# Kernel tuning notes

Measured on AMD Instinct MI355X. Metric: run time of the kernel, lower is better.

The kernel has to match this reference:

```python
import jax, jax.numpy as jnp
import numpy as np
import math

B, S, D, H, HD = 2, 2048, 2048, 16, 128
ROPE_THETA = 10000.0


def _rope_cache(seq_len, dim, base, dtype=jnp.float32):
    inv_freq = 1.0 / (base ** (jnp.arange(0, dim, 2, dtype=jnp.float32) / dim))
    t = jnp.arange(seq_len, dtype=jnp.float32)
    freqs = jnp.einsum('i,j->ij', t, inv_freq)          # [S, dim/2]
    emb = jnp.concatenate([freqs, freqs], axis=-1)       # [S, dim]
    return jnp.cos(emb).astype(dtype), jnp.sin(emb).astype(dtype)


def _rotate_half(x):
    x1, x2 = x[..., : x.shape[-1] // 2], x[..., x.shape[-1] // 2:]
    return jnp.concatenate([-x2, x1], axis=-1)


def setup_inputs() -> dict:
    key = jax.random.key(0)
    ks = jax.random.split(key, 6)
    hidden_states = jax.random.normal(ks[0], (B, S, D), dtype=jnp.float32) * 0.02
    w_scale = 1.0 / math.sqrt(D)
    Wq = jax.random.normal(ks[1], (D, D), dtype=jnp.float32) * w_scale
    Wk = jax.random.normal(ks[2], (D, D), dtype=jnp.float32) * w_scale
    Wv = jax.random.normal(ks[3], (D, D), dtype=jnp.float32) * w_scale
    Wo = jax.random.normal(ks[4], (D, D), dtype=jnp.float32) * w_scale
    # additive causal mask [B, 1, S, S]: 0 on/below diag, large negative above
    causal = jnp.tril(jnp.ones((S, S), dtype=bool))
    attention_mask = jnp.where(causal, 0.0, -1e9).astype(jnp.float32)
    attention_mask = jnp.broadcast_to(attention_mask[None, None], (B, 1, S, S))
    position_ids = jnp.broadcast_to(jnp.arange(S, dtype=jnp.int32)[None], (B, S))
    return {
        'hidden_states': hidden_states,
        'attention_mask': attention_mask,
        'position_ids': position_ids,
        'Wq': Wq, 'Wk': Wk, 'Wv': Wv, 'Wo': Wo,
    }


def reference(hidden_states, attention_mask, position_ids, Wq, Wk, Wv, Wo):
    bsz, q_len, _ = hidden_states.shape
    # projections (torch Linear: x @ W.T), then split heads -> [B, H, S, HD]
    def proj(W):
        return jnp.einsum('bsd,ed->bse', hidden_states, W).reshape(bsz, q_len, H, HD).transpose(0, 2, 1, 3)
    q, k, v = proj(Wq), proj(Wk), proj(Wv)
    cos_c, sin_c = _rope_cache(q_len, HD, ROPE_THETA, hidden_states.dtype)
    cos = cos_c[position_ids][:, None]  # [B, 1, S, HD]
    sin = sin_c[position_ids][:, None]
    q = q * cos + _rotate_half(q) * sin
    k = k * cos + _rotate_half(k) * sin
    scores = jnp.einsum('bhqd,bhkd->bhqk', q, k) / math.sqrt(HD)
    scores = scores + attention_mask
    attn_weights = jax.nn.softmax(scores.astype(jnp.float32), axis=-1).astype(q.dtype)
    attn_out = jnp.einsum('bhqk,bhkd->bhqd', attn_weights, v)
    attn_out = attn_out.transpose(0, 2, 1, 3).reshape(bsz, q_len, D)
    out = jnp.einsum('bsd,ed->bse', attn_out, Wo)
    return out
```

## Files before the change

kernel.cpp:

```cpp
#include <hip/hip_runtime.h>

typedef __bf16 bf16;
typedef __bf16 bf16x8 __attribute__((ext_vector_type(8)));
typedef float f32x4 __attribute__((ext_vector_type(4)));

#define D_MODEL 2048
#define SEQ 2048
#define NH 16
#define HEAD_DIM 128
#define NBATCH 2
#define SM_SCALE 0.08838834764831845f
#define WSEG 4194304

typedef __attribute__((address_space(1))) const void* gas_cp;
typedef __attribute__((address_space(3))) void* las_p;
__device__ __forceinline__ void ll16(const bf16* g, bf16* l) {
  __builtin_amdgcn_global_load_lds((gas_cp)g, (las_p)l, 16, 0, 0);
}

__device__ __forceinline__ bf16x8 cvt8(const float* p) {
  float4 a = *(const float4*)p;
  float4 b = *(const float4*)(p + 4);
  bf16x8 v;
  v[0] = (bf16)a.x; v[1] = (bf16)a.y; v[2] = (bf16)a.z; v[3] = (bf16)a.w;
  v[4] = (bf16)b.x; v[5] = (bf16)b.y; v[6] = (bf16)b.z; v[7] = (bf16)b.w;
  return v;
}

__global__ __launch_bounds__(256)
void cvt_hidden(const float* __restrict__ src, bf16* __restrict__ dst) {
  size_t i = ((size_t)blockIdx.x * 256 + threadIdx.x) * 8;
  *(bf16x8*)(dst + i) = cvt8(src + i);
}

__global__ __launch_bounds__(256)
void cvt_weights(const float* __restrict__ w0, const float* __restrict__ w1,
                 const float* __restrict__ w2, const float* __restrict__ w3,
                 bf16* __restrict__ dst) {
  const float* src = (blockIdx.y == 0) ? w0 : (blockIdx.y == 1) ? w1
                   : (blockIdx.y == 2) ? w2 : w3;
  size_t i = ((size_t)blockIdx.x * 256 + threadIdx.x) * 8;
  *(bf16x8*)(dst + (size_t)blockIdx.y * WSEG + i) = cvt8(src + i);
}

template <typename TC, int MODE>
__global__ __launch_bounds__(256)
void gemm_bt(const bf16* __restrict__ A, const bf16* __restrict__ W,
             TC* __restrict__ C, bf16* __restrict__ Qo, bf16* __restrict__ Ko,
             bf16* __restrict__ Vo, const int* __restrict__ pos_ids) {
  __shared__ __align__(16) bf16 As[2 * 128 * 32];
  __shared__ __align__(16) bf16 Bs[2 * 128 * 32];

  const int tid  = threadIdx.x;
  const int lane = tid & 63;
  const int w    = tid >> 6;
  const int quad = lane >> 4, l15 = lane & 15;
  const int mBase = blockIdx.y * 128;
  const int nBase = blockIdx.x * 128;

  const int srow = w * 32 + (lane >> 2);
  const int scol = (lane & 3) * 8;
  const bf16* Ag0 = A + (size_t)(mBase + srow) * D_MODEL + scol;
  const bf16* Ag1 = Ag0 + (size_t)16 * D_MODEL;
  const bf16* Wg0 = W + (size_t)(nBase + srow) * D_MODEL + scol;
  const bf16* Wg1 = Wg0 + (size_t)16 * D_MODEL;
  const int ldsOff = (w * 32) * 32;

  f32x4 acc[2][8];
#pragma unroll
  for (int i = 0; i < 2; i++)
#pragma unroll
    for (int j = 0; j < 8; j++) acc[i][j] = 0.0f;

  ll16(Ag0, As + ldsOff);
  ll16(Ag1, As + ldsOff + 16 * 32);
  ll16(Wg0, Bs + ldsOff);
  ll16(Wg1, Bs + ldsOff + 16 * 32);
  __syncthreads();

  int cur = 0;
  for (int kk = 0; kk < D_MODEL; kk += 32, cur ^= 1) {
    if (kk + 32 < D_MODEL) {
      const int nx = cur ^ 1;
      ll16(Ag0 + kk + 32, As + nx * 4096 + ldsOff);
      ll16(Ag1 + kk + 32, As + nx * 4096 + ldsOff + 16 * 32);
      ll16(Wg0 + kk + 32, Bs + nx * 4096 + ldsOff);
      ll16(Wg1 + kk + 32, Bs + nx * 4096 + ldsOff + 16 * 32);
    }
    const bf16* Afrag = As + cur * 4096 + (w * 32 + l15) * 32 + quad * 8;
    const bf16* Bfrag = Bs + cur * 4096 + l15 * 32 + quad * 8;
    bf16x8 af[2], bfr[8];
#pragma unroll
    for (int mi = 0; mi < 2; mi++) af[mi] = *(const bf16x8*)(Afrag + mi * 16 * 32);
#pragma unroll
    for (int ni = 0; ni < 8; ni++) bfr[ni] = *(const bf16x8*)(Bfrag + ni * 16 * 32);
#pragma unroll
    for (int mi = 0; mi < 2; mi++)
#pragma unroll
      for (int ni = 0; ni < 8; ni++)
        acc[mi][ni] = __builtin_amdgcn_mfma_f32_16x16x32_bf16(af[mi], bfr[ni], acc[mi][ni], 0, 0, 0);
    __syncthreads();
  }

  if (MODE == 0) {
#pragma unroll
    for (int mi = 0; mi < 2; mi++) {
      int m = mBase + w * 32 + mi * 16 + quad * 4;
#pragma unroll
      for (int ni = 0; ni < 8; ni++) {
        int n = nBase + ni * 16 + l15;
        TC* cp = C + (size_t)m * D_MODEL + n;
#pragma unroll
        for (int r = 0; r < 4; r++) cp[(size_t)r * D_MODEL] = (TC)acc[mi][ni][r];
      }
    }
  } else {
    const int matrix = nBase >> 11;
    const int nb     = nBase & 2047;
    if (matrix == 2) {
      const int h = nb >> 7;
#pragma unroll
      for (int mi = 0; mi < 2; mi++) {
#pragma unroll
        for (int ni = 0; ni < 8; ni++) {
          int hd = ni * 16 + l15;
#pragma unroll
          for (int r = 0; r < 4; r++) {
            int m = mBase + w * 32 + mi * 16 + quad * 4 + r;
            int b = m >> 11, s = m & 2047;
            Vo[((size_t)((b * NH + h) * HEAD_DIM + hd)) * SEQ + s] = (bf16)acc[mi][ni][r];
          }
        }
      }
    } else {
      bf16* Out = (matrix == 0) ? Qo : Ko;
      float invf[4];
#pragma unroll
      for (int ni = 0; ni < 4; ni++)
        invf[ni] = __expf(-(float)(ni * 16 + l15) * (9.210340371976184f / 64.0f));
#pragma unroll
      for (int mi = 0; mi < 2; mi++) {
#pragma unroll
        for (int r = 0; r < 4; r++) {
          int m = mBase + w * 32 + mi * 16 + quad * 4 + r;
          float pos = (float)pos_ids[m];
          bf16* op = Out + (size_t)m * D_MODEL + nb;
#pragma unroll
          for (int ni = 0; ni < 4; ni++) {
            float sn, cs;
            __sincosf(pos * invf[ni], &sn, &cs);
            float q0 = acc[mi][ni][r], q1 = acc[mi][ni + 4][r];
            op[ni * 16 + l15]      = (bf16)(q0 * cs - q1 * sn);
            op[ni * 16 + l15 + 64] = (bf16)(q1 * cs + q0 * sn);
          }
        }
      }
    }
  }
}

__global__ __launch_bounds__(256, 3)
void attn_mfma(const bf16* __restrict__ Q, const bf16* __restrict__ K,
               const bf16* __restrict__ Vt, bf16* __restrict__ O) {
  __shared__ __align__(16) bf16 K_lds[64 * 136];
  __shared__ __align__(16) bf16 V_lds[128 * 72];
  __shared__ __align__(16) bf16 P_lds[64 * 72];

  const int tid  = threadIdx.x;
  const int lane = tid & 63;
  const int w    = tid >> 6;
  const int quad = lane >> 4, l15 = lane & 15;
  const int s    = 31 - blockIdx.y;
  const int bh   = blockIdx.x;
  const size_t qkBase = (size_t)(bh >> 4) * SEQ * D_MODEL + (size_t)(bh & 15) * HEAD_DIM;
  const size_t vBase  = (size_t)bh * HEAD_DIM * SEQ;

  const int qbase = s * 64 + w * 16;

  bf16x8 qa[4];
#pragma unroll
  for (int kk = 0; kk < 4; kk++)
    qa[kk] = *(const bf16x8*)(Q + qkBase + (size_t)(qbase + l15) * D_MODEL + kk * 32 + quad * 8);

  bf16x8 ones;
#pragma unroll
  for (int i = 0; i < 8; i++) ones[i] = (bf16)1.0f;

  f32x4 oacc[8], ls;
#pragma unroll
  for (int ni = 0; ni < 8; ni++) oacc[ni] = 0.0f;
  ls = 0.0f;

  const int ntiles = s + 1;

  bf16x8 kr[4], vr[4];
  auto loadKV = [&](int t0) {
#pragma unroll
    for (int i = 0; i < 4; i++) {
      int c = tid + 256 * i;
      kr[i] = *(const bf16x8*)(K + qkBase + (size_t)(t0 + (c >> 4)) * D_MODEL + (c & 15) * 8);
    }
#pragma unroll
    for (int i = 0; i < 4; i++) {
      int c = tid + 256 * i;
      vr[i] = *(const bf16x8*)(Vt + vBase + (size_t)(c >> 3) * SEQ + t0 + (c & 7) * 8);
    }
  };
  loadKV(0);

  const int prow = w * 16;

  for (int tt = 0; tt < ntiles; tt++) {
    const int t0 = tt * 64;
    __syncthreads();
#pragma unroll
    for (int i = 0; i < 4; i++) {
      int c = tid + 256 * i;
      *(bf16x8*)&K_lds[(c >> 4) * 136 + (c & 15) * 8] = kr[i];
    }
#pragma unroll
    for (int i = 0; i < 4; i++) {
      int c = tid + 256 * i;
      *(bf16x8*)&V_lds[(c >> 3) * 72 + (c & 7) * 8] = vr[i];
    }
    __syncthreads();
    if (tt + 1 < ntiles) loadKV(t0 + 64);

    f32x4 sacc[4];
#pragma unroll
    for (int ni = 0; ni < 4; ni++) sacc[ni] = 0.0f;
#pragma unroll
    for (int kk = 0; kk < 4; kk++) {
#pragma unroll
      for (int ni = 0; ni < 4; ni++) {
        bf16x8 kf = *(const bf16x8*)&K_lds[(ni * 16 + l15) * 136 + kk * 32 + quad * 8];
        sacc[ni] = __builtin_amdgcn_mfma_f32_16x16x32_bf16(qa[kk], kf, sacc[ni], 0, 0, 0);
      }
    }

    if (tt == s) {
#pragma unroll
      for (int r = 0; r < 4; r++) {
        int qrow = qbase + quad * 4 + r;
#pragma unroll
        for (int ni = 0; ni < 4; ni++) {
          int tcol = t0 + ni * 16 + l15;
          float pv = (tcol <= qrow) ? __expf(fminf(sacc[ni][r] * SM_SCALE, 30.0f)) : 0.0f;
          P_lds[(prow + quad * 4 + r) * 72 + ni * 16 + l15] = (bf16)pv;
        }
      }
    } else {
#pragma unroll
      for (int r = 0; r < 4; r++)
#pragma unroll
        for (int ni = 0; ni < 4; ni++)
          P_lds[(prow + quad * 4 + r) * 72 + ni * 16 + l15] =
              (bf16)__expf(fminf(sacc[ni][r] * SM_SCALE, 30.0f));
    }

#pragma unroll
    for (int kk2 = 0; kk2 < 2; kk2++) {
      bf16x8 pf = *(const bf16x8*)&P_lds[(prow + l15) * 72 + kk2 * 32 + quad * 8];
#pragma unroll
      for (int ni = 0; ni < 8; ni++) {
        bf16x8 vf = *(const bf16x8*)&V_lds[(ni * 16 + l15) * 72 + kk2 * 32 + quad * 8];
        oacc[ni] = __builtin_amdgcn_mfma_f32_16x16x32_bf16(pf, vf, oacc[ni], 0, 0, 0);
      }
      ls = __builtin_amdgcn_mfma_f32_16x16x32_bf16(pf, ones, ls, 0, 0, 0);
    }
  }

#pragma unroll
  for (int r = 0; r < 4; r++) {
    float inv = 1.0f / ls[r];
    bf16* op = O + qkBase + (size_t)(qbase + quad * 4 + r) * D_MODEL;
#pragma unroll
    for (int ni = 0; ni < 8; ni++)
      op[ni * 16 + l15] = (bf16)(oacc[ni][r] * inv);
  }
}

extern "C" void kernel_launch(void* const* d_in, const int* in_sizes, int n_in,
                              void* d_out, int out_size, void* d_ws, size_t ws_size,
                              hipStream_t stream) {
  const float* hidden = (const float*)d_in[0];
  const int* pos = (const int*)d_in[2];
  const float* Wq = (const float*)d_in[3];
  const float* Wk = (const float*)d_in[4];
  const float* Wv = (const float*)d_in[5];
  const float* Wo = (const float*)d_in[6];
  float* out = (float*)d_out;

  const size_t TENS = (size_t)NBATCH * SEQ * D_MODEL;
  bf16* Qb = (bf16*)d_ws;
  bf16* Kb = Qb + TENS;
  bf16* Vt = Kb + TENS;
  bf16* AO = Vt + TENS;
  bf16* Hb = AO + TENS;
  bf16* Wb = Hb + TENS;

  dim3 blk(256);
  cvt_hidden<<<dim3(TENS / 2048), blk, 0, stream>>>(hidden, Hb);
  cvt_weights<<<dim3(WSEG / 2048, 4), blk, 0, stream>>>(Wq, Wk, Wv, Wo, Wb);

  gemm_bt<bf16, 1><<<dim3(48, 32), blk, 0, stream>>>(
      Hb, Wb, (bf16*)nullptr, Qb, Kb, Vt, pos);

  attn_mfma<<<dim3(NBATCH * NH, 32), blk, 0, stream>>>(Qb, Kb, Vt, AO);

  gemm_bt<float, 0><<<dim3(16, 32), blk, 0, stream>>>(
      AO, Wb + 3 * (size_t)WSEG, out, nullptr, nullptr, nullptr, nullptr);
}
```

Before: 420.8 us.

## Replace GEMM with 256x256-tile 8-wave four-phase pipelined kernel

Replaces the 128x128, 4-wave double-buffered GEMM with a 256x256-tile, 512-thread kernel. Each K=64 step is split into four quadrant phases that interleave LDS fragment loads, async global-to-LDS staging for later tiles, barriers and priority-raised MFMA bursts. It also XOR-swizzles the LDS layout to avoid bank conflicts and remaps block IDs for L2 locality. The aim is more data reuse per tile and overlap of memory and compute, at the cost of 128KB LDS per block, fewer blocks (384 and 128), and fragile hand-scheduled waitcnt logic.

```diff
diff --git a/kernel.cpp b/kernel.cpp
--- a/kernel.cpp
+++ b/kernel.cpp
@@ -11,6 +11,7 @@
 #define NBATCH 2
 #define SM_SCALE 0.08838834764831845f
 #define WSEG 4194304
+#define NT_TILES 32
 
 typedef __attribute__((address_space(1))) const void* gas_cp;
 typedef __attribute__((address_space(3))) void* las_p;
@@ -43,118 +44,205 @@
   *(bf16x8*)(dst + (size_t)blockIdx.y * WSEG + i) = cvt8(src + i);
 }
 
-template <typename TC, int MODE>
-__global__ __launch_bounds__(256)
-void gemm_bt(const bf16* __restrict__ A, const bf16* __restrict__ W,
-             TC* __restrict__ C, bf16* __restrict__ Qo, bf16* __restrict__ Ko,
-             bf16* __restrict__ Vo, const int* __restrict__ pos_ids) {
-  __shared__ __align__(16) bf16 As[2 * 128 * 32];
-  __shared__ __align__(16) bf16 Bs[2 * 128 * 32];
+#define LOADA(HB)                                                            \
+  _Pragma("unroll") for (int mi = 0; mi < 2; mi++)                           \
+  _Pragma("unroll") for (int ks = 0; ks < 2; ks++)                           \
+      af[mi][ks] = *(const bf16x8*)((HB) + ((rowA + mi * 16) << 7) +         \
+                                    (ks ? kx1 : kx0));
+
+#define LOADB(HB)                                                            \
+  _Pragma("unroll") for (int ks = 0; ks < 2; ks++) {                         \
+    bfr[0][ks] = *(const bf16x8*)((HB) + (rb0 << 7) + (ks ? kx1 : kx0));     \
+    bfr[1][ks] = *(const bf16x8*)((HB) + (rb1 << 7) + (ks ? kx1 : kx0));     \
+    bfr[2][ks] = *(const bf16x8*)((HB) + (rb2 << 7) + (ks ? kx1 : kx0));     \
+    bfr[3][ks] = *(const bf16x8*)((HB) + (rb3 << 7) + (ks ? kx1 : kx0));     \
+  }
+
+#define MMAC(QM, QN)                                                         \
+  _Pragma("unroll") for (int ks = 0; ks < 2; ks++)                           \
+  _Pragma("unroll") for (int mi = 0; mi < 2; mi++)                           \
+  _Pragma("unroll") for (int ni = 0; ni < 4; ni++)                           \
+      acc[QM][QN][mi][ni] = __builtin_amdgcn_mfma_f32_16x16x32_bf16(         \
+          af[mi][ks], bfr[ni][ks], acc[QM][QN][mi][ni], 0, 0, 0);
+
+#define STAGE(GP, ROW0, KT, LB)                                              \
+  _Pragma("unroll") for (int i_ = 0; i_ < 2; i_++) {                         \
+    ll16((GP) + (size_t)((ROW0) + (i_ * 8 + w) * 8 + l8) * D_MODEL +         \
+             (KT) * 64 + kelem,                                              \
+         (bf16*)((LB) + (i_ * 8 + w) * 1024));                               \
+  }
+
+#define PHASE_SYNC_PRE()                                                     \
+  __builtin_amdgcn_s_barrier();                                              \
+  asm volatile("s_waitcnt lgkmcnt(0)" ::: "memory");                         \
+  __builtin_amdgcn_sched_barrier(0);                                         \
+  __builtin_amdgcn_s_setprio(1);
+
+#define PHASE_SYNC_POST()                                                    \
+  __builtin_amdgcn_s_setprio(0);                                             \
+  __builtin_amdgcn_s_barrier();
+
+template <typename TC, int MODE, int NBN>
+__global__ __launch_bounds__(512, 2)
+void gemm8p(const bf16* __restrict__ A, const bf16* __restrict__ W,
+            TC* __restrict__ C, bf16* __restrict__ Qo, bf16* __restrict__ Ko,
+            bf16* __restrict__ Vo, const int* __restrict__ pos_ids) {
+  __shared__ __align__(16) char smem[131072];
 
   const int tid  = threadIdx.x;
   const int lane = tid & 63;
   const int w    = tid >> 6;
   const int quad = lane >> 4, l15 = lane & 15;
-  const int mBase = blockIdx.y * 128;
-  const int nBase = blockIdx.x * 128;
-
-  const int srow = w * 32 + (lane >> 2);
-  const int scol = (lane & 3) * 8;
-  const bf16* Ag0 = A + (size_t)(mBase + srow) * D_MODEL + scol;
-  const bf16* Ag1 = Ag0 + (size_t)16 * D_MODEL;
-  const bf16* Wg0 = W + (size_t)(nBase + srow) * D_MODEL + scol;
-  const bf16* Wg1 = Wg0 + (size_t)16 * D_MODEL;
-  const int ldsOff = (w * 32) * 32;
-
-  f32x4 acc[2][8];
-#pragma unroll
-  for (int i = 0; i < 2; i++)
-#pragma unroll
-    for (int j = 0; j < 8; j++) acc[i][j] = 0.0f;
-
-  ll16(Ag0, As + ldsOff);
-  ll16(Ag1, As + ldsOff + 16 * 32);
-  ll16(Wg0, Bs + ldsOff);
-  ll16(Wg1, Bs + ldsOff + 16 * 32);
-  __syncthreads();
-
-  int cur = 0;
-  for (int kk = 0; kk < D_MODEL; kk += 32, cur ^= 1) {
-    if (kk + 32 < D_MODEL) {
-      const int nx = cur ^ 1;
-      ll16(Ag0 + kk + 32, As + nx * 4096 + ldsOff);
-      ll16(Ag1 + kk + 32, As + nx * 4096 + ldsOff + 16 * 32);
-      ll16(Wg0 + kk + 32, Bs + nx * 4096 + ldsOff);
-      ll16(Wg1 + kk + 32, Bs + nx * 4096 + ldsOff + 16 * 32);
-    }
-    const bf16* Afrag = As + cur * 4096 + (w * 32 + l15) * 32 + quad * 8;
-    const bf16* Bfrag = Bs + cur * 4096 + l15 * 32 + quad * 8;
-    bf16x8 af[2], bfr[8];
-#pragma unroll
-    for (int mi = 0; mi < 2; mi++) af[mi] = *(const bf16x8*)(Afrag + mi * 16 * 32);
-#pragma unroll
-    for (int ni = 0; ni < 8; ni++) bfr[ni] = *(const bf16x8*)(Bfrag + ni * 16 * 32);
-#pragma unroll
-    for (int mi = 0; mi < 2; mi++)
-#pragma unroll
-      for (int ni = 0; ni < 8; ni++)
-        acc[mi][ni] = __builtin_amdgcn_mfma_f32_16x16x32_bf16(af[mi], bfr[ni], acc[mi][ni], 0, 0, 0);
-    __syncthreads();
+  const int wr   = w >> 1;
+  const int wc   = w & 1;
+  const int l8   = lane >> 3, l7 = lane & 7;
+  const int kelem = 8 * (l7 ^ l8);
+
+  const int nwg = 16 * NBN;
+  const int bid = blockIdx.x;
+  const int lin = (bid & 7) * (nwg >> 3) + (bid >> 3);
+  const int by = lin / NBN, bx = lin % NBN;
+  const int mBase = by << 8, nBase = bx << 8;
+
+  const int kx0 = (quad * 16) ^ ((l15 & 7) << 4);
+  const int kx1 = kx0 ^ 64;
+  const int rowA = wr * 32 + l15;
+  const int rb0 = wc * 32 + l15, rb1 = rb0 + 16, rb2 = rb0 + 64, rb3 = rb0 + 80;
+
+  f32x4 acc[2][2][2][4];
+#pragma unroll
+  for (int a = 0; a < 2; a++)
+#pragma unroll
+    for (int b = 0; b < 2; b++)
+#pragma unroll
+      for (int c = 0; c < 2; c++)
+#pragma unroll
+        for (int d = 0; d < 4; d++) acc[a][b][c][d] = 0.0f;
+
+  bf16x8 af[2][2], bfr[4][2];
+
+  {
+    char* s = smem;
+    STAGE(A, mBase,       0, s + 0);
+    STAGE(A, mBase + 128, 0, s + 16384);
+    STAGE(W, nBase,       0, s + 32768);
+    STAGE(W, nBase + 128, 0, s + 49152);
+    STAGE(W, nBase,       1, s + 65536 + 32768);
+    STAGE(A, mBase + 128, 1, s + 65536 + 16384);
+  }
+  asm volatile("s_waitcnt vmcnt(4)" ::: "memory");
+  __builtin_amdgcn_s_barrier();
+
+  for (int t = 0; t < NT_TILES; ++t) {
+    const int buf = t & 1;
+    char* const A0  = smem + buf * 65536;
+    char* const A1h = A0 + 16384;
+    char* const B0  = A0 + 32768;
+    char* const B1h = B0 + 16384;
+    char* const oA0 = smem + (buf ^ 1) * 65536;
+    char* const oB1 = oA0 + 32768 + 16384;
+
+    LOADA(A0);
+    LOADB(B0);
+    if (t + 1 < NT_TILES) STAGE(A, mBase, t + 1, oA0);
+    PHASE_SYNC_PRE();
+    MMAC(0, 0);
+    PHASE_SYNC_POST();
+
+    LOADA(A1h);
+    if (t + 1 < NT_TILES) STAGE(W, nBase + 128, t + 1, oB1);
+    PHASE_SYNC_PRE();
+    MMAC(1, 0);
+    PHASE_SYNC_POST();
+
+    LOADB(B1h);
+    if (t + 2 < NT_TILES) STAGE(W, nBase, t + 2, B0);
+    PHASE_SYNC_PRE();
+    MMAC(1, 1);
+    PHASE_SYNC_POST();
+
+    LOADA(A0);
+    if (t + 2 < NT_TILES) STAGE(A, mBase + 128, t + 2, A1h);
+    __builtin_amdgcn_s_barrier();
+    asm volatile("s_waitcnt lgkmcnt(0)" ::: "memory");
+    __builtin_amdgcn_sched_barrier(0);
+    __builtin_amdgcn_s_setprio(1);
+    MMAC(0, 1);
+    __builtin_amdgcn_s_setprio(0);
+    if (t + 2 < NT_TILES)
+      asm volatile("s_waitcnt vmcnt(4)" ::: "memory");
+    else
+      asm volatile("s_waitcnt vmcnt(0)" ::: "memory");
+    __builtin_amdgcn_s_barrier();
   }
 
   if (MODE == 0) {
 #pragma unroll
-    for (int mi = 0; mi < 2; mi++) {
-      int m = mBase + w * 32 + mi * 16 + quad * 4;
-#pragma unroll
-      for (int ni = 0; ni < 8; ni++) {
-        int n = nBase + ni * 16 + l15;
-        TC* cp = C + (size_t)m * D_MODEL + n;
-#pragma unroll
-        for (int r = 0; r < 4; r++) cp[(size_t)r * D_MODEL] = (TC)acc[mi][ni][r];
-      }
-    }
+    for (int qm = 0; qm < 2; qm++)
+#pragma unroll
+      for (int qn = 0; qn < 2; qn++)
+#pragma unroll
+        for (int mi = 0; mi < 2; mi++)
+#pragma unroll
+          for (int ni = 0; ni < 4; ni++) {
+            int n = nBase + qn * 128 + wc * 32 + (ni & 1) * 16 + (ni >> 1) * 64 + l15;
+            int mb = mBase + qm * 128 + wr * 32 + mi * 16 + quad * 4;
+            TC* cp = C + (size_t)mb * D_MODEL + n;
+#pragma unroll
+            for (int r = 0; r < 4; r++) cp[(size_t)r * D_MODEL] = (TC)acc[qm][qn][mi][ni][r];
+          }
   } else {
     const int matrix = nBase >> 11;
     const int nb     = nBase & 2047;
     if (matrix == 2) {
-      const int h = nb >> 7;
-#pragma unroll
-      for (int mi = 0; mi < 2; mi++) {
-#pragma unroll
-        for (int ni = 0; ni < 8; ni++) {
-          int hd = ni * 16 + l15;
-#pragma unroll
-          for (int r = 0; r < 4; r++) {
-            int m = mBase + w * 32 + mi * 16 + quad * 4 + r;
-            int b = m >> 11, s = m & 2047;
-            Vo[((size_t)((b * NH + h) * HEAD_DIM + hd)) * SEQ + s] = (bf16)acc[mi][ni][r];
-          }
+#pragma unroll
+      for (int qm = 0; qm < 2; qm++)
+#pragma unroll
+        for (int qn = 0; qn < 2; qn++) {
+          const int h = (nb >> 7) + qn;
+#pragma unroll
+          for (int mi = 0; mi < 2; mi++)
+#pragma unroll
+            for (int ni = 0; ni < 4; ni++) {
+              const int hd = wc * 32 + (ni & 1) * 16 + (ni >> 1) * 64 + l15;
+#pragma unroll
+              for (int r = 0; r < 4; r++) {
+                int m = mBase + qm * 128 + wr * 32 + mi * 16 + quad * 4 + r;
+                int b = m >> 11, s2 = m & 2047;
+                Vo[((size_t)((b * NH + h) * HEAD_DIM + hd)) * SEQ + s2] =
+                    (bf16)acc[qm][qn][mi][ni][r];
+              }
+            }
         }
-      }
     } else {
       bf16* Out = (matrix == 0) ? Qo : Ko;
-      float invf[4];
-#pragma unroll
-      for (int ni = 0; ni < 4; ni++)
-        invf[ni] = __expf(-(float)(ni * 16 + l15) * (9.210340371976184f / 64.0f));
-#pragma unroll
-      for (int mi = 0; mi < 2; mi++) {
-#pragma unroll
-        for (int r = 0; r < 4; r++) {
-          int m = mBase + w * 32 + mi * 16 + quad * 4 + r;
-          float pos = (float)pos_ids[m];
-          bf16* op = Out + (size_t)m * D_MODEL + nb;
-#pragma unroll
-          for (int ni = 0; ni < 4; ni++) {
-            float sn, cs;
-            __sincosf(pos * invf[ni], &sn, &cs);
-            float q0 = acc[mi][ni][r], q1 = acc[mi][ni + 4][r];
-            op[ni * 16 + l15]      = (bf16)(q0 * cs - q1 * sn);
-            op[ni * 16 + l15 + 64] = (bf16)(q1 * cs + q0 * sn);
+      float invf[2];
+#pragma unroll
+      for (int ni = 0; ni < 2; ni++)
+        invf[ni] = __expf(-(float)(wc * 32 + ni * 16 + l15) *
+                          (9.210340371976184f / 64.0f));
+#pragma unroll
+      for (int qm = 0; qm < 2; qm++)
+#pragma unroll
+        for (int mi = 0; mi < 2; mi++)
+#pragma unroll
+          for (int r = 0; r < 4; r++) {
+            int m = mBase + qm * 128 + wr * 32 + mi * 16 + quad * 4 + r;
+            float pos = (float)pos_ids[m];
+#pragma unroll
+            for (int qn = 0; qn < 2; qn++) {
+              bf16* op = Out + (size_t)m * D_MODEL + nb + qn * 128 + wc * 32 + l15;
+#pragma unroll
+              for (int ni = 0; ni < 2; ni++) {
+                float sn, cs;
+                __sincosf(pos * invf[ni], &sn, &cs);
+                float q0 = acc[qm][qn][mi][ni][r];
+                float q1 = acc[qm][qn][mi][ni + 2][r];
+                op[ni * 16]      = (bf16)(q0 * cs - q1 * sn);
+                op[ni * 16 + 64] = (bf16)(q1 * cs + q0 * sn);
+              }
+            }
           }
-        }
-      }
     }
   }
 }
@@ -299,15 +387,14 @@
   bf16* Hb = AO + TENS;
   bf16* Wb = Hb + TENS;
 
-  dim3 blk(256);
-  cvt_hidden<<<dim3(TENS / 2048), blk, 0, stream>>>(hidden, Hb);
-  cvt_weights<<<dim3(WSEG / 2048, 4), blk, 0, stream>>>(Wq, Wk, Wv, Wo, Wb);
-
-  gemm_bt<bf16, 1><<<dim3(48, 32), blk, 0, stream>>>(
+  cvt_hidden<<<dim3(TENS / 2048), dim3(256), 0, stream>>>(hidden, Hb);
+  cvt_weights<<<dim3(WSEG / 2048, 4), dim3(256), 0, stream>>>(Wq, Wk, Wv, Wo, Wb);
+
+  gemm8p<bf16, 1, 24><<<dim3(384), dim3(512), 0, stream>>>(
       Hb, Wb, (bf16*)nullptr, Qb, Kb, Vt, pos);
 
-  attn_mfma<<<dim3(NBATCH * NH, 32), blk, 0, stream>>>(Qb, Kb, Vt, AO);
-
-  gemm_bt<float, 0><<<dim3(16, 32), blk, 0, stream>>>(
+  attn_mfma<<<dim3(NBATCH * NH, 32), dim3(256), 0, stream>>>(Qb, Kb, Vt, AO);
+
+  gemm8p<float, 0, 8><<<dim3(128), dim3(512), 0, stream>>>(
       AO, Wb + 3 * (size_t)WSEG, out, nullptr, nullptr, nullptr, nullptr);
 }
```

Result: faster. 389.0 us (-7.5%).
